# Kernel tuning notes

Hardware: AMD Instinct MI355X
Metric: run time of the kernel (lower is better)

The kernel has to match this reference:

```python
import jax, jax.numpy as jnp
import numpy as np

DIM = 768
NUM_HEADS = 12
HEAD_DIM = DIM // NUM_HEADS
SCALE = HEAD_DIM ** (-0.5)
WH, WW = 14, 14
NUM_EXTRA = 1
NUM_REL_DIST = (2 * WH - 1) * (2 * WW - 1) + NUM_EXTRA * (NUM_EXTRA + 2)  # 732
N_TOK = WH * WW + NUM_EXTRA  # 197
BATCH = 64


def make_rel_pos_index():
    # mirrors the torch buffer construction (meshgrid 'ij')
    coords = np.stack(np.meshgrid(np.arange(WH), np.arange(WW), indexing='ij'))  # [2,Wh,Ww]
    coords_flat = coords.reshape(2, -1)  # [2, Wh*Ww]
    rel = coords_flat[:, :, None] - coords_flat[:, None, :]  # [2, M, M]
    rel = rel.transpose(1, 2, 0).astype(np.int64)  # [M, M, 2]
    rel[:, :, 0] += WH - 1
    rel[:, :, 1] += WW - 1
    rel[:, :, 0] *= 2 * WW - 1
    idx = np.zeros((N_TOK, N_TOK), dtype=np.int64)
    idx[NUM_EXTRA:, NUM_EXTRA:] = rel.sum(-1)
    idx[0, 0:] = NUM_REL_DIST - 3
    idx[0:, 0] = NUM_REL_DIST - 2
    idx[0, 0] = NUM_REL_DIST - 1
    return jnp.asarray(idx, dtype=jnp.int32)


def setup_inputs() -> dict:
    key = jax.random.key(0)
    ks = jax.random.split(key, 7)
    x = jax.random.normal(ks[0], (BATCH, N_TOK, DIM), dtype=jnp.float32)
    qkv_w = jax.random.normal(ks[1], (3 * DIM, DIM), dtype=jnp.float32) * (DIM ** -0.5)
    q_bias = jax.random.normal(ks[2], (DIM,), dtype=jnp.float32) * 0.02
    v_bias = jax.random.normal(ks[3], (DIM,), dtype=jnp.float32) * 0.02
    rpb_table = jax.random.normal(ks[4], (NUM_REL_DIST, NUM_HEADS), dtype=jnp.float32) * 0.02
    proj_w = jax.random.normal(ks[5], (DIM, DIM), dtype=jnp.float32) * (DIM ** -0.5)
    proj_b = jax.random.normal(ks[6], (DIM,), dtype=jnp.float32) * 0.02
    rel_index = make_rel_pos_index()
    return {"x": x, "qkv_w": qkv_w, "q_bias": q_bias, "v_bias": v_bias,
            "rpb_table": rpb_table, "proj_w": proj_w, "proj_b": proj_b,
            "rel_index": rel_index}


def reference(x, qkv_w, q_bias, v_bias, rpb_table, proj_w, proj_b, rel_index):
    B, N, C = x.shape
    # qkv bias: [q_bias, zeros, v_bias]
    qkv_bias = jnp.concatenate([q_bias, jnp.zeros_like(v_bias), v_bias]).astype(x.dtype)
    qkv = x @ qkv_w.T + qkv_bias  # [B,N,3C]
    qkv = qkv.reshape(B, N, 3, NUM_HEADS, HEAD_DIM).transpose(2, 0, 3, 1, 4)  # [3,B,H,N,d]
    q, k, v = qkv[0] * SCALE, qkv[1], qkv[2]
    # fp32 scores, as in the original
    attn = jnp.einsum('bhnd,bhmd->bhnm', q.astype(jnp.float32), k.astype(jnp.float32))
    # relative position bias gather: [N,N,H] -> [H,N,N]
    bias = rpb_table[rel_index.reshape(-1)].reshape(N, N, NUM_HEADS).transpose(2, 0, 1)
    attn = jax.nn.softmax(attn + bias[None].astype(jnp.float32), axis=-1)
    out = jnp.einsum('bhnm,bhmd->bhnd', attn, v.astype(attn.dtype))
    out = out.transpose(0, 2, 1, 3).reshape(B, N, -1).astype(x.dtype)
    return out @ proj_w.T + proj_b
```

## Files before the change

kernel.cpp:

```cpp
#include <hip/hip_runtime.h>
#include <hip/hip_bf16.h>

#define DIM 768
#define NHEADS 12
#define HD 64
#define NTOK 197
#define BATCH 64
#define NTOKENS (BATCH*NTOK)
#define NPAIR (NTOK*NTOK)
#define QK_SCALE 0.125f
#define CDIM 2304

typedef short bf16x8 __attribute__((ext_vector_type(8)));
typedef float f32x4 __attribute__((ext_vector_type(4)));

#define MFMA(a,b,c) __builtin_amdgcn_mfma_f32_16x16x32_bf16(a,b,c,0,0,0)

__device__ __forceinline__ unsigned short f2bf(float f) {
    union { float f; unsigned u; } v; v.f = f;
    unsigned r = v.u + 0x7FFFu + ((v.u >> 16) & 1u);
    return (unsigned short)(r >> 16);
}

__device__ __forceinline__ void gload16(const unsigned short* g, unsigned short* l) {
    __builtin_amdgcn_global_load_lds(
        (const __attribute__((address_space(1))) void*)g,
        (__attribute__((address_space(3))) void*)l, 16, 0, 0);
}

__device__ __forceinline__ int xcd_swz(int orig, int nwg) {
    int q = nwg >> 3, r = nwg & 7;
    int xcd = orig & 7, idx = orig >> 3;
    return (xcd < r ? xcd * (q + 1) : r * (q + 1) + (xcd - r) * q) + idx;
}

#define NB_X 4728
#define NB_WQ 864
#define NB_WP 288
#define NB_BIAS 1820

__device__ __forceinline__ void cvt8(const float* __restrict__ s,
                                     unsigned short* __restrict__ d, int t, int n8) {
    if (t >= n8) return;
    float4 a = ((const float4*)s)[t * 2], b = ((const float4*)s)[t * 2 + 1];
    union { unsigned short u[8]; bf16x8 v; } p;
    p.u[0] = f2bf(a.x); p.u[1] = f2bf(a.y); p.u[2] = f2bf(a.z); p.u[3] = f2bf(a.w);
    p.u[4] = f2bf(b.x); p.u[5] = f2bf(b.y); p.u[6] = f2bf(b.z); p.u[7] = f2bf(b.w);
    ((bf16x8*)d)[t] = p.v;
}

__global__ __launch_bounds__(256) void prep(
    const float* __restrict__ x, const float* __restrict__ qw,
    const float* __restrict__ pw, const float* __restrict__ rpb,
    const int* __restrict__ rel,
    unsigned short* __restrict__ Xb, unsigned short* __restrict__ Wqb,
    unsigned short* __restrict__ Wpb, float* __restrict__ biasm)
{
    int bid = blockIdx.x;
    if (bid < NB_X) {
        cvt8(x, Xb, bid * 256 + threadIdx.x, NB_X * 256);
    } else if (bid < NB_X + NB_WQ) {
        cvt8(qw, Wqb, (bid - NB_X) * 256 + threadIdx.x, NB_WQ * 256);
    } else if (bid < NB_X + NB_WQ + NB_WP) {
        cvt8(pw, Wpb, (bid - NB_X - NB_WQ) * 256 + threadIdx.x, NB_WP * 256);
    } else {
        int t = (bid - NB_X - NB_WQ - NB_WP) * 256 + threadIdx.x;
        if (t < NHEADS * NPAIR) {
            int h = t / NPAIR, p = t - h * NPAIR;
            biasm[t] = rpb[rel[p] * NHEADS + h];
        }
    }
}

#define NKT 12
#define TMAX 6
#define BUFE 16384

#define LDA(bo, mh) do { _Pragma("unroll") for (int mi = 0; mi < 4; ++mi) { \
    af[mi][0] = *(const bf16x8*)&AsF[(bo) + abase0 + ((mh)*4+mi)*1024 + sl0*8]; \
    af[mi][1] = *(const bf16x8*)&AsF[(bo) + abase0 + ((mh)*4+mi)*1024 + sl1*8]; } } while(0)
#define LDB(bo, nh) do { _Pragma("unroll") for (int ni = 0; ni < 2; ++ni) { \
    bw[ni][0] = *(const bf16x8*)&BsF[(bo) + bbase0 + ((nh)*2+ni)*1024 + sl0*8]; \
    bw[ni][1] = *(const bf16x8*)&BsF[(bo) + bbase0 + ((nh)*2+ni)*1024 + sl1*8]; } } while(0)
#define MM(mh, nh) do { __builtin_amdgcn_s_setprio(1); \
    _Pragma("unroll") for (int mi = 0; mi < 4; ++mi) \
    _Pragma("unroll") for (int ni = 0; ni < 2; ++ni) { \
        acc[(mh)*4+mi][(nh)*2+ni] = MFMA(af[mi][0], bw[ni][0], acc[(mh)*4+mi][(nh)*2+ni]); \
        acc[(mh)*4+mi][(nh)*2+ni] = MFMA(af[mi][1], bw[ni][1], acc[(mh)*4+mi][(nh)*2+ni]); } \
    __builtin_amdgcn_s_setprio(0); } while(0)
#define SA(Ap, buf, h, kt) do { \
    gload16(Ap + asrc[2*(h)] + (kt)*64, &AsF[(buf)*BUFE + adoff[2*(h)]]); \
    gload16(Ap + asrc[2*(h)+1] + (kt)*64, &AsF[(buf)*BUFE + adoff[2*(h)+1]]); } while(0)
#define SB(Bp, buf, h, kt) do { \
    gload16(Bp + bsrc[2*(h)] + (kt)*64, &BsF[(buf)*BUFE + adoff[2*(h)]]); \
    gload16(Bp + bsrc[2*(h)+1] + (kt)*64, &BsF[(buf)*BUFE + adoff[2*(h)+1]]); } while(0)
#define BAR __builtin_amdgcn_s_barrier()
#define WVM0 asm volatile("s_waitcnt vmcnt(0)" ::: "memory")

#define KLOOP(Ap, Bp) \
    SA(Ap, 0, 0, 0); SA(Ap, 0, 1, 0); SB(Bp, 0, 0, 0); SB(Bp, 0, 1, 0); \
    WVM0; BAR; \
    for (int t = 0; t < TMAX; ++t) { \
        int k1 = 2 * t + 1, k2 = 2 * t + 2; \
        bool st = (t < TMAX - 1); \
        LDA(0, 0); LDB(0, 0); SA(Ap, 1, 0, k1);            BAR; MM(0, 0); BAR; \
        LDB(0, 1);            SA(Ap, 1, 1, k1);            BAR; MM(0, 1); BAR; \
        LDA(0, 1);            SB(Bp, 1, 0, k1);            BAR; MM(1, 1); BAR; \
        LDB(0, 0);            SB(Bp, 1, 1, k1);            BAR; MM(1, 0); WVM0; BAR; \
        LDA(BUFE, 0); LDB(BUFE, 0); if (st) SA(Ap, 0, 0, k2); BAR; MM(0, 0); BAR; \
        LDB(BUFE, 1);               if (st) SA(Ap, 0, 1, k2); BAR; MM(0, 1); BAR; \
        LDA(BUFE, 1);               if (st) SB(Bp, 0, 0, k2); BAR; MM(1, 1); BAR; \
        LDB(BUFE, 0);               if (st) SB(Bp, 0, 1, k2); BAR; MM(1, 0); \
        if (st) { WVM0; } BAR; \
    }

__global__ __launch_bounds__(512, 2) void gemm_qkv8(
    const unsigned short* __restrict__ Xb, const unsigned short* __restrict__ Wb,
    const float* __restrict__ qbias, const float* __restrict__ vbias,
    unsigned short* __restrict__ QKVb)
{
    __shared__ __attribute__((aligned(16))) unsigned short AsF[2 * BUFE];
    __shared__ __attribute__((aligned(16))) unsigned short BsF[2 * BUFE];
    int tid = threadIdx.x, lane = tid & 63, wid = tid >> 6;
    int wr = wid >> 2, wc = wid & 3;
    int wg = xcd_swz(blockIdx.x, 450);
    int bx = wg / 9, by = wg % 9;
    int m0 = bx * 256, n0 = by * 256;
    int r15 = lane & 15, hi = lane >> 4, sx = lane & 7;
    int sl0 = hi ^ sx, sl1 = (hi + 4) ^ sx;

    size_t asrc[4], bsrc[4];
    int adoff[4];
    #pragma unroll
    for (int i = 0; i < 4; ++i) {
        int c = i * 512 + tid;
        int row = c >> 3, s = c & 7, rr = row & 127, half = row >> 7;
        int slot = s ^ (rr & 7);
        int ar = m0 + row; if (ar >= NTOKENS) ar = NTOKENS - 1;
        asrc[i] = (size_t)ar * DIM + slot * 8;
        bsrc[i] = (size_t)(n0 + row) * DIM + slot * 8;
        adoff[i] = half * 8192 + rr * 64 + s * 8;
    }
    int abase0 = wr * 8192 + r15 * 64;
    int bbase0 = (wc >> 1) * 8192 + (wc & 1) * 4096 + r15 * 64;

    f32x4 acc[8][4];
    #pragma unroll
    for (int i = 0; i < 8; ++i)
        #pragma unroll
        for (int j = 0; j < 4; ++j) acc[i][j] = (f32x4){0.f, 0.f, 0.f, 0.f};

    bf16x8 af[4][2], bw[2][2];
    KLOOP(Xb, Wb)

    unsigned short* reg = (wid < 4) ? &AsF[wid * 8192] : &BsF[(wid - 4) * 8192];
    {
        int which = n0 / DIM;
        float scl = (which == 0) ? QK_SCALE : 1.f;
        #pragma unroll
        for (int n = 0; n < 4; ++n) {
            int colr = n0 - which * DIM + wc * 64 + n * 16 + r15;
            float bv = (which == 0) ? qbias[colr] : (which == 2 ? vbias[colr] : 0.f);
            #pragma unroll
            for (int m = 0; m < 8; ++m) {
                int lrb = m * 16 + hi * 4;
                #pragma unroll
                for (int r = 0; r < 4; ++r) {
                    int lr = lrb + r;
                    int c = n * 16 + r15;
                    reg[lr * 64 + (c ^ (((lr >> 2) & 3) << 4))] =
                        f2bf((acc[m][n][r] + bv) * scl);
                }
            }
        }
    }
    #pragma unroll
    for (int it = 0; it < 16; ++it) {
        int c = it * 64 + lane;
        int lr = c >> 3, cc = c & 7;
        int row = m0 + wr * 128 + lr;
        if (row < NTOKENS) {
            bf16x8 v = *(bf16x8*)&reg[lr * 64 + ((cc * 8) ^ (((lr >> 2) & 3) << 4))];
            *(bf16x8*)(QKVb + (size_t)row * CDIM + n0 + wc * 64 + cc * 8) = v;
        }
    }
}

__global__ __launch_bounds__(512, 2) void gemm_proj8(
    const unsigned short* __restrict__ Ob, const unsigned short* __restrict__ Wp,
    const float* __restrict__ pbias, float* __restrict__ out)
{
    __shared__ __attribute__((aligned(16))) unsigned short AsF[2 * BUFE];
    __shared__ __attribute__((aligned(16))) unsigned short BsF[2 * BUFE];
    int tid = threadIdx.x, lane = tid & 63, wid = tid >> 6;
    int wr = wid >> 2, wc = wid & 3;
    int wg = xcd_swz(blockIdx.x, 150);
    int bx = wg / 3, by = wg % 3;
    int m0 = bx * 256, n0 = by * 256;
    int r15 = lane & 15, hi = lane >> 4, sx = lane & 7;
    int sl0 = hi ^ sx, sl1 = (hi + 4) ^ sx;

    size_t asrc[4], bsrc[4];
    int adoff[4];
    #pragma unroll
    for (int i = 0; i < 4; ++i) {
        int c = i * 512 + tid;
        int row = c >> 3, s = c & 7, rr = row & 127, half = row >> 7;
        int slot = s ^ (rr & 7);
        int ar = m0 + row; if (ar >= NTOKENS) ar = NTOKENS - 1;
        asrc[i] = (size_t)ar * DIM + slot * 8;
        bsrc[i] = (size_t)(n0 + row) * DIM + slot * 8;
        adoff[i] = half * 8192 + rr * 64 + s * 8;
    }
    int abase0 = wr * 8192 + r15 * 64;
    int bbase0 = (wc >> 1) * 8192 + (wc & 1) * 4096 + r15 * 64;

    f32x4 acc[8][4];
    #pragma unroll
    for (int i = 0; i < 8; ++i)
        #pragma unroll
        for (int j = 0; j < 4; ++j) acc[i][j] = (f32x4){0.f, 0.f, 0.f, 0.f};

    bf16x8 af[4][2], bw[2][2];
    KLOOP(Ob, Wp)

    #pragma unroll
    for (int n = 0; n < 4; ++n) {
        int col = n0 + wc * 64 + n * 16 + r15;
        float bv = pbias[col];
        #pragma unroll
        for (int m = 0; m < 8; ++m) {
            #pragma unroll
            for (int r = 0; r < 4; ++r) {
                int row = m0 + wr * 128 + m * 16 + hi * 4 + r;
                if (row < NTOKENS)
                    out[(size_t)row * DIM + col] = acc[m][n][r] + bv;
            }
        }
    }
}

#define KP 72
#define PP 232
#define VPITCH 256

__global__ __launch_bounds__(256, 2) void attn(
    const unsigned short* __restrict__ QKV, const float* __restrict__ biasm,
    unsigned short* __restrict__ O)
{
    __shared__ __attribute__((aligned(16))) unsigned short VT[64 * VPITCH];
    __shared__ __attribute__((aligned(16))) unsigned short KlPl[208 * KP];

    int tid = threadIdx.x, lane = tid & 63, wid = tid >> 6;
    int r15 = lane & 15, hi = lane >> 4;
    int wg = blockIdx.x;
    int g = wg >> 5, qt = (wg >> 3) & 3, p = wg & 7;
    int bh = g * 8 + p;
    int h = bh % NHEADS, b = bh / NHEADS;
    size_t tb = (size_t)b * NTOK;
    int hq = h * 64;
    int rbase = qt * 64 + wid * 16 + hi * 4;

    int kcol = (tid & 7) * 8;
    bf16x8 kreg[7];
    #pragma unroll
    for (int t = 0; t < 7; ++t) {
        int row = t * 32 + (tid >> 3);
        int rc = row < NTOK ? row : (NTOK - 1);
        kreg[t] = *(const bf16x8*)(QKV + (tb + rc) * CDIM + 768 + hq + kcol);
    }
    #pragma unroll
    for (int t = 0; t < 7; ++t) {
        int row = t * 32 + (tid >> 3);
        if (row < NTOK)
            *(bf16x8*)&KlPl[row * KP + kcol] = kreg[t];
    }

    bf16x8 v0r[4], v1r[4];
    #pragma unroll
    for (int it = 0; it < 4; ++it) {
        int c = it * 256 + tid;
        int rp = c >> 3, kc = c & 7;
        int r0 = 2 * rp, r1 = 2 * rp + 1;
        bf16x8 z = (bf16x8)(short)0;
        v0r[it] = z; v1r[it] = z;
        if (r0 < NTOK) v0r[it] = *(const bf16x8*)(QKV + (tb + r0) * CDIM + 1536 + hq + kc * 8);
        if (r1 < NTOK) v1r[it] = *(const bf16x8*)(QKV + (tb + r1) * CDIM + 1536 + hq + kc * 8);
    }

    int qrow_g = qt * 64 + wid * 16 + r15;
    int qsrc = qrow_g < NTOK ? qrow_g : (NTOK - 1);
    bf16x8 aq[2];
    #pragma unroll
    for (int ks = 0; ks < 2; ++ks)
        aq[ks] = *(const bf16x8*)(QKV + (tb + qsrc) * CDIM + hq + ks * 32 + hi * 8);

    float breg[4][13];
    {
        const float* bb = biasm + h * NPAIR;
        #pragma unroll
        for (int r = 0; r < 4; ++r) {
            int row_g = rbase + r;
            int rowc = row_g < NTOK ? row_g : (NTOK - 1);
            const float* brow = bb + rowc * NTOK + r15;
            #pragma unroll
            for (int t = 0; t < 13; ++t) {
                int off = t * 16;
                if (t == 12 && r15 >= 5) off = 0;
                breg[r][t] = brow[off];
            }
        }
    }
    __syncthreads();

    f32x4 sa[13];
    #pragma unroll
    for (int t = 0; t < 13; ++t) sa[t] = (f32x4){0.f,0.f,0.f,0.f};
    __builtin_amdgcn_s_setprio(1);
    #pragma unroll
    for (int t = 0; t < 13; ++t) {
        #pragma unroll
        for (int ks = 0; ks < 2; ++ks) {
            bf16x8 bk = *(bf16x8*)&KlPl[(t * 16 + r15) * KP + ks * 32 + hi * 8];
            sa[t] = MFMA(aq[ks], bk, sa[t]);
        }
    }
    __builtin_amdgcn_s_setprio(0);
    __syncthreads();

    #pragma unroll
    for (int it = 0; it < 4; ++it) {
        int c = it * 256 + tid;
        int rp = c >> 3, kc = c & 7;
        if (rp < 112) {
            #pragma unroll
            for (int j = 0; j < 8; ++j) {
                unsigned int w = (unsigned int)(unsigned short)v0r[it][j] |
                                 ((unsigned int)(unsigned short)v1r[it][j] << 16);
                int slot2 = (rp >> 2) ^ j ^ kc;
                *(unsigned int*)&VT[(kc * 8 + j) * VPITCH + slot2 * 8 + (rp & 3) * 2] = w;
            }
        }
    }

    int plbase = wid * (16 * PP);
    float invr[4];
    #pragma unroll
    for (int r = 0; r < 4; ++r) {
        #pragma unroll
        for (int t = 0; t < 13; ++t) {
            int col = t * 16 + r15;
            if (col < NTOK) sa[t][r] += breg[r][t];
            else            sa[t][r] = -1e30f;
        }
        float mx = sa[0][r];
        #pragma unroll
        for (int t = 1; t < 13; ++t) mx = fmaxf(mx, sa[t][r]);
        #pragma unroll
        for (int m = 1; m < 16; m <<= 1) mx = fmaxf(mx, __shfl_xor(mx, m));
        float sum = 0.f;
        #pragma unroll
        for (int t = 0; t < 13; ++t) {
            float e = __expf(sa[t][r] - mx);
            sa[t][r] = e; sum += e;
        }
        int roff = plbase + (hi * 4 + r) * PP;
        #pragma unroll
        for (int t = 0; t < 13; ++t)
            KlPl[roff + t * 16 + r15] = f2bf(sa[t][r]);
        KlPl[roff + 208 + r15] = 0;
        #pragma unroll
        for (int m = 1; m < 16; m <<= 1) sum += __shfl_xor(sum, m);
        invr[r] = __builtin_amdgcn_rcpf(sum);
    }
    __syncthreads();

    f32x4 oa[4];
    #pragma unroll
    for (int dt = 0; dt < 4; ++dt) oa[dt] = (f32x4){0.f,0.f,0.f,0.f};
    int X = hi ^ (r15 & 7) ^ (r15 >> 3);
    __builtin_amdgcn_s_setprio(1);
    #pragma unroll
    for (int ks = 0; ks < 7; ++ks) {
        bf16x8 ap = *(bf16x8*)&KlPl[plbase + r15 * PP + ks * 32 + hi * 8];
        #pragma unroll
        for (int dt = 0; dt < 4; ++dt) {
            int d = dt * 16 + r15;
            int slotp = (ks * 4) ^ (dt * 2) ^ X;
            bf16x8 bv = *(bf16x8*)&VT[d * VPITCH + slotp * 8];
            oa[dt] = MFMA(ap, bv, oa[dt]);
        }
    }
    __builtin_amdgcn_s_setprio(0);

    #pragma unroll
    for (int dt = 0; dt < 4; ++dt)
        #pragma unroll
        for (int r = 0; r < 4; ++r)
            KlPl[plbase + (hi * 4 + r) * 72 + dt * 16 + r15] = f2bf(oa[dt][r] * invr[r]);
    #pragma unroll
    for (int it = 0; it < 2; ++it) {
        int c = it * 64 + lane;
        int lr = c >> 3, cc = c & 7;
        int qrow = qt * 64 + wid * 16 + lr;
        if (qrow < NTOK)
            *(bf16x8*)(O + (tb + qrow) * DIM + hq + cc * 8) =
                *(bf16x8*)&KlPl[plbase + lr * 72 + cc * 8];
    }
}

extern "C" void kernel_launch(void* const* d_in, const int* in_sizes, int n_in,
                              void* d_out, int out_size, void* d_ws, size_t ws_size,
                              hipStream_t stream) {
    const float* x      = (const float*)d_in[0];
    const float* qkv_w  = (const float*)d_in[1];
    const float* q_bias = (const float*)d_in[2];
    const float* v_bias = (const float*)d_in[3];
    const float* rpb    = (const float*)d_in[4];
    const float* proj_w = (const float*)d_in[5];
    const float* proj_b = (const float*)d_in[6];
    const int*   rel    = (const int*)d_in[7];
    float* out = (float*)d_out;

    const size_t NELEM = (size_t)NTOKENS * DIM;
    const size_t WQKV  = (size_t)3 * DIM * DIM;
    const size_t WPROJ = (size_t)DIM * DIM;
    unsigned short* Xb   = (unsigned short*)d_ws;
    unsigned short* Wqb  = Xb + NELEM;
    unsigned short* Wpb  = Wqb + WQKV;
    unsigned short* QKVb = Wpb + WPROJ;
    float* biasm = (float*)(QKVb + (size_t)NTOKENS * CDIM);
    unsigned short* Ob = Xb;

    prep<<<NB_X + NB_WQ + NB_WP + NB_BIAS, 256, 0, stream>>>(
        x, qkv_w, proj_w, rpb, rel, Xb, Wqb, Wpb, biasm);

    gemm_qkv8<<<450, 512, 0, stream>>>(Xb, Wqb, q_bias, v_bias, QKVb);

    attn<<<3072, 256, 0, stream>>>(QKVb, biasm, Ob);

    gemm_proj8<<<150, 512, 0, stream>>>(Ob, Wpb, proj_b, out);
}
```

Baseline: 166.3 us.

## Store relative-position bias as bf16 and retile projection GEMM to 128x128

The relative-position bias matrix is now stored in bf16 instead of fp32, halving its footprint and the attention kernel's bias reads. The projection GEMM drops the 256x256 tile, 512-thread pipelined kernel for a simpler 128x128 tile, 256-thread kernel with a single-buffered LDS loop, launching 594 blocks instead of 150 so more CUs are occupied. The cost is lost double-buffering overlap in the projection and a small precision loss in the bias values.

```diff
diff --git a/kernel.cpp b/kernel.cpp
--- a/kernel.cpp
+++ b/kernel.cpp
@@ -22,6 +22,10 @@
     return (unsigned short)(r >> 16);
 }
 
+__device__ __forceinline__ float bf2f(unsigned short u) {
+    union { unsigned v; float f; } x; x.v = ((unsigned)u) << 16; return x.f;
+}
+
 __device__ __forceinline__ void gload16(const unsigned short* g, unsigned short* l) {
     __builtin_amdgcn_global_load_lds(
         (const __attribute__((address_space(1))) void*)g,
@@ -54,7 +58,7 @@
     const float* __restrict__ pw, const float* __restrict__ rpb,
     const int* __restrict__ rel,
     unsigned short* __restrict__ Xb, unsigned short* __restrict__ Wqb,
-    unsigned short* __restrict__ Wpb, float* __restrict__ biasm)
+    unsigned short* __restrict__ Wpb, unsigned short* __restrict__ biasm)
 {
     int bid = blockIdx.x;
     if (bid < NB_X) {
@@ -67,7 +71,7 @@
         int t = (bid - NB_X - NB_WQ - NB_WP) * 256 + threadIdx.x;
         if (t < NHEADS * NPAIR) {
             int h = t / NPAIR, p = t - h * NPAIR;
-            biasm[t] = rpb[rel[p] * NHEADS + h];
+            biasm[t] = f2bf(rpb[rel[p] * NHEADS + h]);
         }
     }
 }
@@ -186,55 +190,83 @@
     }
 }
 
-__global__ __launch_bounds__(512, 2) void gemm_proj8(
+__global__ __launch_bounds__(256, 2) void gemm_proj(
     const unsigned short* __restrict__ Ob, const unsigned short* __restrict__ Wp,
     const float* __restrict__ pbias, float* __restrict__ out)
 {
-    __shared__ __attribute__((aligned(16))) unsigned short AsF[2 * BUFE];
-    __shared__ __attribute__((aligned(16))) unsigned short BsF[2 * BUFE];
+    __shared__ __attribute__((aligned(16))) unsigned short As[128 * 64];
+    __shared__ __attribute__((aligned(16))) unsigned short Bs[128 * 64];
     int tid = threadIdx.x, lane = tid & 63, wid = tid >> 6;
-    int wr = wid >> 2, wc = wid & 3;
-    int wg = xcd_swz(blockIdx.x, 150);
-    int bx = wg / 3, by = wg % 3;
-    int m0 = bx * 256, n0 = by * 256;
+    int wg = xcd_swz(blockIdx.x, 594);
+    int bx = wg / 6, by = wg % 6;
+    int m0 = bx * 128, n0 = by * 128;
+    int wm = (wid >> 1) * 64, wn = (wid & 1) * 64;
+
+    size_t abase[4], bbase[4];
+    unsigned short *alds[4], *blds[4];
+    #pragma unroll
+    for (int i = 0; i < 4; ++i) {
+        int chunk = i * 4 + wid;
+        int row = chunk * 8 + (lane >> 3);
+        int slot = (lane & 7) ^ (row & 7);
+        int ar = m0 + row; if (ar >= NTOKENS) ar = NTOKENS - 1;
+        abase[i] = (size_t)ar * DIM + slot * 8;
+        bbase[i] = (size_t)(n0 + row) * DIM + slot * 8;
+        alds[i] = &As[chunk * 512];
+        blds[i] = &Bs[chunk * 512];
+    }
     int r15 = lane & 15, hi = lane >> 4, sx = lane & 7;
-    int sl0 = hi ^ sx, sl1 = (hi + 4) ^ sx;
-
-    size_t asrc[4], bsrc[4];
-    int adoff[4];
+    int s0 = (hi ^ sx) * 8, s1 = ((hi + 4) ^ sx) * 8;
+    int arow[4], brow[4];
     #pragma unroll
     for (int i = 0; i < 4; ++i) {
-        int c = i * 512 + tid;
-        int row = c >> 3, s = c & 7, rr = row & 127, half = row >> 7;
-        int slot = s ^ (rr & 7);
-        int ar = m0 + row; if (ar >= NTOKENS) ar = NTOKENS - 1;
-        asrc[i] = (size_t)ar * DIM + slot * 8;
-        bsrc[i] = (size_t)(n0 + row) * DIM + slot * 8;
-        adoff[i] = half * 8192 + rr * 64 + s * 8;
-    }
-    int abase0 = wr * 8192 + r15 * 64;
-    int bbase0 = (wc >> 1) * 8192 + (wc & 1) * 4096 + r15 * 64;
-
-    f32x4 acc[8][4];
-    #pragma unroll
-    for (int i = 0; i < 8; ++i)
+        arow[i] = (wm + i * 16 + r15) * 64;
+        brow[i] = (wn + i * 16 + r15) * 64;
+    }
+
+    f32x4 acc[4][4];
+    #pragma unroll
+    for (int i = 0; i < 4; ++i)
         #pragma unroll
         for (int j = 0; j < 4; ++j) acc[i][j] = (f32x4){0.f, 0.f, 0.f, 0.f};
 
-    bf16x8 af[4][2], bw[2][2];
-    KLOOP(Ob, Wp)
-
-    #pragma unroll
-    for (int n = 0; n < 4; ++n) {
-        int col = n0 + wc * 64 + n * 16 + r15;
+    for (int k0 = 0; k0 < DIM; k0 += 64) {
+        __syncthreads();
+        #pragma unroll
+        for (int i = 0; i < 4; ++i) {
+            gload16(Ob + abase[i] + k0, alds[i]);
+            gload16(Wp + bbase[i] + k0, blds[i]);
+        }
+        __syncthreads();
+        #pragma unroll
+        for (int ks = 0; ks < 2; ++ks) {
+            int so = ks ? s1 : s0;
+            bf16x8 af[4], bwv[4];
+            #pragma unroll
+            for (int i = 0; i < 4; ++i) af[i] = *(bf16x8*)&As[arow[i] + so];
+            #pragma unroll
+            for (int j = 0; j < 4; ++j) bwv[j] = *(bf16x8*)&Bs[brow[j] + so];
+            __builtin_amdgcn_s_setprio(1);
+            #pragma unroll
+            for (int i = 0; i < 4; ++i)
+                #pragma unroll
+                for (int j = 0; j < 4; ++j)
+                    acc[i][j] = MFMA(af[i], bwv[j], acc[i][j]);
+            __builtin_amdgcn_s_setprio(0);
+        }
+    }
+
+    #pragma unroll
+    for (int j = 0; j < 4; ++j) {
+        int col = n0 + wn + j * 16 + r15;
         float bv = pbias[col];
         #pragma unroll
-        for (int m = 0; m < 8; ++m) {
+        for (int i = 0; i < 4; ++i) {
             #pragma unroll
             for (int r = 0; r < 4; ++r) {
-                int row = m0 + wr * 128 + m * 16 + hi * 4 + r;
+                int row = m0 + wm + i * 16 + hi * 4 + r;
                 if (row < NTOKENS)
-                    out[(size_t)row * DIM + col] = acc[m][n][r] + bv;
+                    out[(size_t)row * DIM + col] = acc[i][j][r] + bv;
             }
         }
     }
@@ -245,7 +277,7 @@
 #define VPITCH 256
 
 __global__ __launch_bounds__(256, 2) void attn(
-    const unsigned short* __restrict__ QKV, const float* __restrict__ biasm,
+    const unsigned short* __restrict__ QKV, const unsigned short* __restrict__ biasm,
     unsigned short* __restrict__ O)
 {
     __shared__ __attribute__((aligned(16))) unsigned short VT[64 * VPITCH];
@@ -295,14 +327,14 @@
     for (int ks = 0; ks < 2; ++ks)
         aq[ks] = *(const bf16x8*)(QKV + (tb + qsrc) * CDIM + hq + ks * 32 + hi * 8);
 
-    float breg[4][13];
+    unsigned short breg[4][13];
     {
-        const float* bb = biasm + h * NPAIR;
+        const unsigned short* bb = biasm + h * NPAIR;
         #pragma unroll
         for (int r = 0; r < 4; ++r) {
             int row_g = rbase + r;
             int rowc = row_g < NTOK ? row_g : (NTOK - 1);
-            const float* brow = bb + rowc * NTOK + r15;
+            const unsigned short* brow = bb + rowc * NTOK + r15;
             #pragma unroll
             for (int t = 0; t < 13; ++t) {
                 int off = t * 16;
@@ -350,7 +382,7 @@
         #pragma unroll
         for (int t = 0; t < 13; ++t) {
             int col = t * 16 + r15;
-            if (col < NTOK) sa[t][r] += breg[r][t];
+            if (col < NTOK) sa[t][r] += bf2f(breg[r][t]);
             else            sa[t][r] = -1e30f;
         }
         float mx = sa[0][r];
@@ -429,7 +461,7 @@
     unsigned short* Wqb  = Xb + NELEM;
     unsigned short* Wpb  = Wqb + WQKV;
     unsigned short* QKVb = Wpb + WPROJ;
-    float* biasm = (float*)(QKVb + (size_t)NTOKENS * CDIM);
+    unsigned short* biasm = QKVb + (size_t)NTOKENS * CDIM;
     unsigned short* Ob = Xb;
 
     prep<<<NB_X + NB_WQ + NB_WP + NB_BIAS, 256, 0, stream>>>(
@@ -439,5 +471,5 @@
 
     attn<<<3072, 256, 0, stream>>>(QKVb, biasm, Ob);
 
-    gemm_proj8<<<150, 512, 0, stream>>>(Ob, Wpb, proj_b, out);
-}
+    gemm_proj<<<594, 256, 0, stream>>>(Ob, Wpb, proj_b, out);
+}
```

Result: faster. 151.4 us (-9.0%).
